# Kernel tuning notes

Hardware: AMD Instinct MI355X
Metric: run time of the kernel (lower is better)

## Reference

```python
import jax, jax.numpy as jnp
import numpy as np

B, P, N, C = 8, 4, 512, 768
H = 12
HD = C // H  # 64
SCALE = HD ** -0.5


def setup_inputs() -> dict:
    key = jax.random.key(0)
    k1, k2, k3 = jax.random.split(key, 3)
    x = jax.random.normal(k1, (B, P, N, C), dtype=jnp.float32)
    W_qkv = jax.random.normal(k2, (3 * C, C), dtype=jnp.float32) * (C ** -0.5)
    W_proj = jax.random.normal(k3, (C, C), dtype=jnp.float32) * (C ** -0.5)
    b_proj = jnp.zeros((C,), dtype=jnp.float32)
    return {"x": x, "W_qkv": W_qkv, "W_proj": W_proj, "b_proj": b_proj}


def reference(x, W_qkv, W_proj, b_proj):
    b, p, n, c = x.shape
    # qkv projection (no bias): (B,P,N,3C) -> (B,P,N,3,H,HD)
    qkv = jnp.einsum('bpnc,dc->bpnd', x, W_qkv).reshape(b, p, n, 3, H, HD)
    # -> (3, B, P, H, N, HD)
    qkv = jnp.transpose(qkv, (3, 0, 1, 4, 2, 5))
    q, k, v = qkv[0], qkv[1], qkv[2]
    # scaled dot-product attention per (batch, patch, head)
    attn = jnp.einsum('bphnd,bphmd->bphnm', q * SCALE, k)
    attn = jax.nn.softmax(attn, axis=-1)
    out = jnp.einsum('bphnm,bphmd->bphnd', attn, v)
    # merge heads: (B,P,N,H,HD) -> (B,P,N,C)
    out = jnp.transpose(out, (0, 1, 3, 2, 4)).reshape(b, p, n, c)
    return jnp.einsum('bpnc,dc->bpnd', out, W_proj) + b_proj
```

## Files before the change

kernel.cpp:

```cpp
#include <hip/hip_runtime.h>

typedef __bf16 bf16x8 __attribute__((ext_vector_type(8)));
typedef unsigned short u16x8 __attribute__((ext_vector_type(8)));
typedef float f32x4 __attribute__((ext_vector_type(4)));

#define GLOAD_LDS16(GP, LP)                                                        \
  __builtin_amdgcn_global_load_lds((const __attribute__((address_space(1))) void*)(GP), \
                                   (__attribute__((address_space(3))) void*)(LP), 16, 0, 0)

__device__ __forceinline__ unsigned short f2bf(float f) {
  unsigned int u = __builtin_bit_cast(unsigned int, f);
  u += 0x7FFFu + ((u >> 16) & 1u);
  return (unsigned short)(u >> 16);
}
__device__ __forceinline__ bf16x8 ldfrag(const unsigned short* p) {
  return __builtin_bit_cast(bf16x8, *(const u16x8*)p);
}
__device__ __forceinline__ f32x4 mfma16(bf16x8 a, bf16x8 b, f32x4 c) {
  return __builtin_amdgcn_mfma_f32_16x16x32_bf16(a, b, c, 0, 0, 0);
}

#define MTOK   16384
#define CDIM   768
#define C3     2304
#define C2     1536
#define NX     12582912
#define NQW    1769472
#define NPW    589824

#define XB_OFF    0ul
#define WQKV_OFF  25165824ul
#define WPROJ_OFF 28704768ul
#define QK_OFF    29884416ul
#define VT_OFF    80216064ul

__global__ __launch_bounds__(256) void convert_kernel(
    const float* __restrict__ x, const float* __restrict__ wqkv,
    const float* __restrict__ wproj, unsigned short* __restrict__ xb,
    unsigned short* __restrict__ wqkvb, unsigned short* __restrict__ wprojb) {
  const int NX4 = NX / 4, NQ4 = NQW / 4, NP4 = NPW / 4;
  const int total = NX4 + NQ4 + NP4;
  for (int i = blockIdx.x * 256 + threadIdx.x; i < total; i += gridDim.x * 256) {
    const float4* src; unsigned short* dst; float scale = 1.f; int j;
    if (i < NX4) { src = (const float4*)x; dst = xb; j = i; }
    else if (i < NX4 + NQ4) {
      j = i - NX4; src = (const float4*)wqkv; dst = wqkvb;
      int d = (j * 4) / CDIM; if (d < CDIM) scale = 0.125f;
    } else { j = i - NX4 - NQ4; src = (const float4*)wproj; dst = wprojb; }
    float4 v = src[j];
    unsigned int lo = f2bf(v.x * scale) | ((unsigned)f2bf(v.y * scale) << 16);
    unsigned int hi = f2bf(v.z * scale) | ((unsigned)f2bf(v.w * scale) << 16);
    uint2 pk; pk.x = lo; pk.y = hi;
    *(uint2*)(dst + (long)j * 4) = pk;
  }
}

template <int MODE>
__global__ __launch_bounds__(256) void gemm_bt(
    const unsigned short* __restrict__ A, const unsigned short* __restrict__ B,
    int K, int Nout,
    unsigned short* __restrict__ out_qk, unsigned short* __restrict__ out_vT,
    float* __restrict__ out_f32, const float* __restrict__ bias) {
  __shared__ unsigned short As[128 * 32];
  __shared__ unsigned short Bs[128 * 32];
  const int tid = threadIdx.x;
  const int wave = tid >> 6, lane = tid & 63;
  const int wy = wave >> 1, wx = wave & 1;
  const int l15 = lane & 15, quad = lane >> 4;
  const int bm = blockIdx.x, bn = blockIdx.y;

  f32x4 acc[4][4];
  for (int i = 0; i < 4; i++)
    for (int j = 0; j < 4; j++) acc[i][j] = f32x4{0.f, 0.f, 0.f, 0.f};

  const long Abase = (long)bm * 128 * K;
  const long Bbase = (long)bn * 128 * K;

  for (int kk = 0; kk < K; kk += 32) {
    for (int i = 0; i < 2; i++) {
      int c = wave * 128 + i * 64 + lane;
      int row = c >> 2, c16 = c & 3;
      GLOAD_LDS16(A + Abase + (long)row * K + kk + c16 * 8, As + c * 8);
      GLOAD_LDS16(B + Bbase + (long)row * K + kk + c16 * 8, Bs + c * 8);
    }
    __syncthreads();
    bf16x8 af[4], bfr[4];
    for (int mt = 0; mt < 4; mt++) af[mt]  = ldfrag(As + (wy * 64 + mt * 16 + l15) * 32 + quad * 8);
    for (int nt = 0; nt < 4; nt++) bfr[nt] = ldfrag(Bs + (wx * 64 + nt * 16 + l15) * 32 + quad * 8);
    for (int mt = 0; mt < 4; mt++)
      for (int nt = 0; nt < 4; nt++)
        acc[mt][nt] = mfma16(af[mt], bfr[nt], acc[mt][nt]);
    __syncthreads();
  }

  if (MODE == 0) {
    if (bn < 12) {
      for (int mt = 0; mt < 4; mt++) {
        int mg = bm * 128 + wy * 64 + mt * 16 + quad * 4;
        for (int nt = 0; nt < 4; nt++) {
          int d = bn * 128 + wx * 64 + nt * 16 + l15;
          for (int r = 0; r < 4; r++)
            out_qk[(long)(mg + r) * C2 + d] = f2bf(acc[mt][nt][r]);
        }
      }
    } else {
      for (int mt = 0; mt < 4; mt++) {
        int mg = bm * 128 + wy * 64 + mt * 16 + quad * 4;
        int bp = mg >> 9, n0 = mg & 511;
        for (int nt = 0; nt < 4; nt++) {
          int dp = bn * 128 - C2 + wx * 64 + nt * 16 + l15;
          int hh = dp >> 6, e = dp & 63;
          unsigned int lo = f2bf(acc[mt][nt][0]) | ((unsigned)f2bf(acc[mt][nt][1]) << 16);
          unsigned int hi = f2bf(acc[mt][nt][2]) | ((unsigned)f2bf(acc[mt][nt][3]) << 16);
          uint2 pk; pk.x = lo; pk.y = hi;
          *(uint2*)(out_vT + ((long)((bp * 12 + hh) * 64 + e) * 512 + n0)) = pk;
        }
      }
    }
  } else {
    for (int nt = 0; nt < 4; nt++) {
      int d = bn * 128 + wx * 64 + nt * 16 + l15;
      float bv = bias[d];
      for (int mt = 0; mt < 4; mt++) {
        int mg = bm * 128 + wy * 64 + mt * 16 + quad * 4;
        for (int r = 0; r < 4; r++)
          out_f32[(long)(mg + r) * Nout + d] = acc[mt][nt][r] + bv;
      }
    }
  }
}

__global__ __launch_bounds__(256) void attn_kernel(
    const unsigned short* __restrict__ qk, const unsigned short* __restrict__ vT,
    unsigned short* __restrict__ aout) {
  const int bph = blockIdx.x;
  const int qt  = blockIdx.y;
  const int bp = bph / 12, h = bph % 12;
  const int tid = threadIdx.x;
  const int wave = tid >> 6, lane = tid & 63;
  const int l15 = lane & 15, quad = lane >> 4;

  __shared__ unsigned short Qs[128 * 72];
  __shared__ unsigned short Ks[64 * 72];
  __shared__ unsigned short Vs[64 * 72];
  __shared__ unsigned short Ps[4 * 32 * 72];

  const unsigned short* Qg = qk + (long)(bp * 512 + qt * 128) * C2 + h * 64;
  const unsigned short* Kg = qk + (long)(bp * 512) * C2 + CDIM + h * 64;
  const unsigned short* Vg = vT + (long)(bp * 12 + h) * 64 * 512;

  for (int i = 0; i < 4; i++) {
    int c = tid + i * 256;
    int row = c >> 3, c8 = c & 7;
    *(uint4*)(Qs + row * 72 + c8 * 8) = *(const uint4*)(Qg + (long)row * C2 + c8 * 8);
  }

  f32x4 o[2][4];
  float mrow[2][4], lrow[2][4];
  for (int a = 0; a < 2; a++)
    for (int b = 0; b < 4; b++) o[a][b] = f32x4{0.f, 0.f, 0.f, 0.f};
  for (int a = 0; a < 2; a++)
    for (int r = 0; r < 4; r++) { mrow[a][r] = -1e30f; lrow[a][r] = 0.f; }

  for (int ch = 0; ch < 8; ch++) {
    if (ch) __syncthreads();
    for (int i = 0; i < 2; i++) {
      int c = tid + i * 256;
      int row = c >> 3, c8 = c & 7;
      *(uint4*)(Ks + row * 72 + c8 * 8) = *(const uint4*)(Kg + (long)(ch * 64 + row) * C2 + c8 * 8);
      *(uint4*)(Vs + row * 72 + c8 * 8) = *(const uint4*)(Vg + (long)row * 512 + ch * 64 + c8 * 8);
    }
    __syncthreads();

    f32x4 s[2][4];
    for (int a = 0; a < 2; a++)
      for (int b = 0; b < 4; b++) s[a][b] = f32x4{0.f, 0.f, 0.f, 0.f};
    for (int ks = 0; ks < 2; ks++) {
      bf16x8 a0 = ldfrag(Qs + (wave * 32 +      l15) * 72 + ks * 32 + quad * 8);
      bf16x8 a1 = ldfrag(Qs + (wave * 32 + 16 + l15) * 72 + ks * 32 + quad * 8);
      for (int nt = 0; nt < 4; nt++) {
        bf16x8 kb = ldfrag(Ks + (nt * 16 + l15) * 72 + ks * 32 + quad * 8);
        s[0][nt] = mfma16(a0, kb, s[0][nt]);
        s[1][nt] = mfma16(a1, kb, s[1][nt]);
      }
    }

    for (int mt2 = 0; mt2 < 2; mt2++) {
      for (int r = 0; r < 4; r++) {
        float mx = fmaxf(fmaxf(s[mt2][0][r], s[mt2][1][r]), fmaxf(s[mt2][2][r], s[mt2][3][r]));
        for (int off = 1; off < 16; off <<= 1) mx = fmaxf(mx, __shfl_xor(mx, off));
        float mnew = fmaxf(mrow[mt2][r], mx);
        float alpha = __expf(mrow[mt2][r] - mnew);
        mrow[mt2][r] = mnew;
        float rs = 0.f;
        for (int nt = 0; nt < 4; nt++) {
          float p = __expf(s[mt2][nt][r] - mnew);
          s[mt2][nt][r] = p;
          rs += p;
        }
        for (int off = 1; off < 16; off <<= 1) rs += __shfl_xor(rs, off);
        lrow[mt2][r] = lrow[mt2][r] * alpha + rs;
        for (int et = 0; et < 4; et++) o[mt2][et][r] *= alpha;
        for (int nt = 0; nt < 4; nt++)
          Ps[(wave * 32 + mt2 * 16 + quad * 4 + r) * 72 + nt * 16 + l15] = f2bf(s[mt2][nt][r]);
      }
    }

    for (int ks = 0; ks < 2; ks++) {
      bf16x8 p0 = ldfrag(Ps + (wave * 32 +      l15) * 72 + ks * 32 + quad * 8);
      bf16x8 p1 = ldfrag(Ps + (wave * 32 + 16 + l15) * 72 + ks * 32 + quad * 8);
      for (int et = 0; et < 4; et++) {
        bf16x8 vb = ldfrag(Vs + (et * 16 + l15) * 72 + ks * 32 + quad * 8);
        o[0][et] = mfma16(p0, vb, o[0][et]);
        o[1][et] = mfma16(p1, vb, o[1][et]);
      }
    }
  }

  for (int mt2 = 0; mt2 < 2; mt2++)
    for (int et = 0; et < 4; et++)
      for (int r = 0; r < 4; r++) {
        int nout = qt * 128 + wave * 32 + mt2 * 16 + quad * 4 + r;
        float v = o[mt2][et][r] / lrow[mt2][r];
        aout[(long)(bp * 512 + nout) * CDIM + h * 64 + et * 16 + l15] = f2bf(v);
      }
}

extern "C" void kernel_launch(void* const* d_in, const int* in_sizes, int n_in,
                              void* d_out, int out_size, void* d_ws, size_t ws_size,
                              hipStream_t stream) {
  (void)in_sizes; (void)n_in; (void)out_size; (void)ws_size;
  const float* x     = (const float*)d_in[0];
  const float* wqkv  = (const float*)d_in[1];
  const float* wproj = (const float*)d_in[2];
  const float* bproj = (const float*)d_in[3];
  float* out = (float*)d_out;
  char* ws = (char*)d_ws;

  unsigned short* xb     = (unsigned short*)(ws + XB_OFF);
  unsigned short* wqkvb  = (unsigned short*)(ws + WQKV_OFF);
  unsigned short* wprojb = (unsigned short*)(ws + WPROJ_OFF);
  unsigned short* qkbuf  = (unsigned short*)(ws + QK_OFF);
  unsigned short* vTbuf  = (unsigned short*)(ws + VT_OFF);
  unsigned short* attn_o = xb;

  convert_kernel<<<2048, 256, 0, stream>>>(x, wqkv, wproj, xb, wqkvb, wprojb);
  gemm_bt<0><<<dim3(128, 18), 256, 0, stream>>>(xb, wqkvb, CDIM, C3, qkbuf, vTbuf, nullptr, nullptr);
  attn_kernel<<<dim3(384, 4), 256, 0, stream>>>(qkbuf, vTbuf, attn_o);
  gemm_bt<1><<<dim3(128, 6), 256, 0, stream>>>(attn_o, wprojb, CDIM, CDIM, nullptr, nullptr, out, bproj);
}
```

Measured before the change: 309.1 us.

## Keep attention probabilities in registers via transposed S and 16x16x16 MFMA for PV

Computes S transposed (K as the A operand, Q as B) so each lane owns one query row. The P fragments can then feed the 16x16x16 bf16 MFMA for PV straight from registers, which removes the LDS round trip for P and the 16-lane shuffles in the row reductions. Softmax now uses exp2, with log2(e) folded into the Q weight scale, and the kernel adds a launch-bounds occupancy hint. The cost is running the PV product on the older, narrower MFMA instruction and higher register pressure.

```diff
diff --git a/kernel.cpp b/kernel.cpp
--- a/kernel.cpp
+++ b/kernel.cpp
@@ -2,6 +2,8 @@
 
 typedef __bf16 bf16x8 __attribute__((ext_vector_type(8)));
 typedef unsigned short u16x8 __attribute__((ext_vector_type(8)));
+typedef short s16x4 __attribute__((ext_vector_type(4)));
+typedef unsigned short u16x4 __attribute__((ext_vector_type(4)));
 typedef float f32x4 __attribute__((ext_vector_type(4)));
 
 #define GLOAD_LDS16(GP, LP)                                                        \
@@ -16,8 +18,14 @@
 __device__ __forceinline__ bf16x8 ldfrag(const unsigned short* p) {
   return __builtin_bit_cast(bf16x8, *(const u16x8*)p);
 }
+__device__ __forceinline__ s16x4 ldfrag4(const unsigned short* p) {
+  return __builtin_bit_cast(s16x4, *(const u16x4*)p);
+}
 __device__ __forceinline__ f32x4 mfma16(bf16x8 a, bf16x8 b, f32x4 c) {
   return __builtin_amdgcn_mfma_f32_16x16x32_bf16(a, b, c, 0, 0, 0);
+}
+__device__ __forceinline__ f32x4 mfma1k(s16x4 a, s16x4 b, f32x4 c) {
+  return __builtin_amdgcn_mfma_f32_16x16x16bf16_1k(a, b, c, 0, 0, 0);
 }
 
 #define MTOK   16384
@@ -27,6 +35,8 @@
 #define NX     12582912
 #define NQW    1769472
 #define NPW    589824
+
+#define QSCALE_LOG2E 0.1803368801111204f
 
 #define XB_OFF    0ul
 #define WQKV_OFF  25165824ul
@@ -45,7 +55,7 @@
     if (i < NX4) { src = (const float4*)x; dst = xb; j = i; }
     else if (i < NX4 + NQ4) {
       j = i - NX4; src = (const float4*)wqkv; dst = wqkvb;
-      int d = (j * 4) / CDIM; if (d < CDIM) scale = 0.125f;
+      int d = (j * 4) / CDIM; if (d < CDIM) scale = QSCALE_LOG2E;
     } else { j = i - NX4 - NQ4; src = (const float4*)wproj; dst = wprojb; }
     float4 v = src[j];
     unsigned int lo = f2bf(v.x * scale) | ((unsigned)f2bf(v.y * scale) << 16);
@@ -130,7 +140,7 @@
   }
 }
 
-__global__ __launch_bounds__(256) void attn_kernel(
+__global__ __launch_bounds__(256, 4) void attn_kernel(
     const unsigned short* __restrict__ qk, const unsigned short* __restrict__ vT,
     unsigned short* __restrict__ aout) {
   const int bph = blockIdx.x;
@@ -143,7 +153,6 @@
   __shared__ unsigned short Qs[128 * 72];
   __shared__ unsigned short Ks[64 * 72];
   __shared__ unsigned short Vs[64 * 72];
-  __shared__ unsigned short Ps[4 * 32 * 72];
 
   const unsigned short* Qg = qk + (long)(bp * 512 + qt * 128) * C2 + h * 64;
   const unsigned short* Kg = qk + (long)(bp * 512) * C2 + CDIM + h * 64;
@@ -156,11 +165,11 @@
   }
 
   f32x4 o[2][4];
-  float mrow[2][4], lrow[2][4];
-  for (int a = 0; a < 2; a++)
+  float mrow[2], lrow[2];
+  for (int a = 0; a < 2; a++) {
     for (int b = 0; b < 4; b++) o[a][b] = f32x4{0.f, 0.f, 0.f, 0.f};
-  for (int a = 0; a < 2; a++)
-    for (int r = 0; r < 4; r++) { mrow[a][r] = -1e30f; lrow[a][r] = 0.f; }
+    mrow[a] = -1e30f; lrow[a] = 0.f;
+  }
 
   for (int ch = 0; ch < 8; ch++) {
     if (ch) __syncthreads();
@@ -172,58 +181,65 @@
     }
     __syncthreads();
 
-    f32x4 s[2][4];
+    f32x4 st[2][4];
     for (int a = 0; a < 2; a++)
-      for (int b = 0; b < 4; b++) s[a][b] = f32x4{0.f, 0.f, 0.f, 0.f};
+      for (int b = 0; b < 4; b++) st[a][b] = f32x4{0.f, 0.f, 0.f, 0.f};
     for (int ks = 0; ks < 2; ks++) {
-      bf16x8 a0 = ldfrag(Qs + (wave * 32 +      l15) * 72 + ks * 32 + quad * 8);
-      bf16x8 a1 = ldfrag(Qs + (wave * 32 + 16 + l15) * 72 + ks * 32 + quad * 8);
+      bf16x8 qf[2];
+      qf[0] = ldfrag(Qs + (wave * 32 +      l15) * 72 + ks * 32 + quad * 8);
+      qf[1] = ldfrag(Qs + (wave * 32 + 16 + l15) * 72 + ks * 32 + quad * 8);
       for (int nt = 0; nt < 4; nt++) {
-        bf16x8 kb = ldfrag(Ks + (nt * 16 + l15) * 72 + ks * 32 + quad * 8);
-        s[0][nt] = mfma16(a0, kb, s[0][nt]);
-        s[1][nt] = mfma16(a1, kb, s[1][nt]);
-      }
-    }
-
+        bf16x8 kf = ldfrag(Ks + (nt * 16 + l15) * 72 + ks * 32 + quad * 8);
+        st[0][nt] = mfma16(kf, qf[0], st[0][nt]);
+        st[1][nt] = mfma16(kf, qf[1], st[1][nt]);
+      }
+    }
+
+    s16x4 pf[2][4];
     for (int mt2 = 0; mt2 < 2; mt2++) {
-      for (int r = 0; r < 4; r++) {
-        float mx = fmaxf(fmaxf(s[mt2][0][r], s[mt2][1][r]), fmaxf(s[mt2][2][r], s[mt2][3][r]));
-        for (int off = 1; off < 16; off <<= 1) mx = fmaxf(mx, __shfl_xor(mx, off));
-        float mnew = fmaxf(mrow[mt2][r], mx);
-        float alpha = __expf(mrow[mt2][r] - mnew);
-        mrow[mt2][r] = mnew;
-        float rs = 0.f;
-        for (int nt = 0; nt < 4; nt++) {
-          float p = __expf(s[mt2][nt][r] - mnew);
-          s[mt2][nt][r] = p;
-          rs += p;
+      float mx = -1e30f;
+      for (int nt = 0; nt < 4; nt++)
+        for (int r = 0; r < 4; r++) mx = fmaxf(mx, st[mt2][nt][r]);
+      mx = fmaxf(mx, __shfl_xor(mx, 16));
+      mx = fmaxf(mx, __shfl_xor(mx, 32));
+      float mnew = fmaxf(mrow[mt2], mx);
+      float alpha = __builtin_amdgcn_exp2f(mrow[mt2] - mnew);
+      mrow[mt2] = mnew;
+      float rs = 0.f;
+      for (int nt = 0; nt < 4; nt++) {
+        f32x4 p;
+        for (int r = 0; r < 4; r++) {
+          p[r] = __builtin_amdgcn_exp2f(st[mt2][nt][r] - mnew);
+          rs += p[r];
         }
-        for (int off = 1; off < 16; off <<= 1) rs += __shfl_xor(rs, off);
-        lrow[mt2][r] = lrow[mt2][r] * alpha + rs;
-        for (int et = 0; et < 4; et++) o[mt2][et][r] *= alpha;
-        for (int nt = 0; nt < 4; nt++)
-          Ps[(wave * 32 + mt2 * 16 + quad * 4 + r) * 72 + nt * 16 + l15] = f2bf(s[mt2][nt][r]);
-      }
-    }
-
-    for (int ks = 0; ks < 2; ks++) {
-      bf16x8 p0 = ldfrag(Ps + (wave * 32 +      l15) * 72 + ks * 32 + quad * 8);
-      bf16x8 p1 = ldfrag(Ps + (wave * 32 + 16 + l15) * 72 + ks * 32 + quad * 8);
+        s16x4 pk;
+        for (int r = 0; r < 4; r++) pk[r] = (short)f2bf(p[r]);
+        pf[mt2][nt] = pk;
+      }
+      rs += __shfl_xor(rs, 16);
+      rs += __shfl_xor(rs, 32);
+      lrow[mt2] = lrow[mt2] * alpha + rs;
+      for (int et = 0; et < 4; et++) o[mt2][et] *= alpha;
+    }
+
+    for (int nt = 0; nt < 4; nt++)
       for (int et = 0; et < 4; et++) {
-        bf16x8 vb = ldfrag(Vs + (et * 16 + l15) * 72 + ks * 32 + quad * 8);
-        o[0][et] = mfma16(p0, vb, o[0][et]);
-        o[1][et] = mfma16(p1, vb, o[1][et]);
-      }
-    }
-  }
-
-  for (int mt2 = 0; mt2 < 2; mt2++)
-    for (int et = 0; et < 4; et++)
-      for (int r = 0; r < 4; r++) {
-        int nout = qt * 128 + wave * 32 + mt2 * 16 + quad * 4 + r;
-        float v = o[mt2][et][r] / lrow[mt2][r];
-        aout[(long)(bp * 512 + nout) * CDIM + h * 64 + et * 16 + l15] = f2bf(v);
-      }
+        s16x4 vf = ldfrag4(Vs + (et * 16 + l15) * 72 + nt * 16 + quad * 4);
+        o[0][et] = mfma1k(vf, pf[0][nt], o[0][et]);
+        o[1][et] = mfma1k(vf, pf[1][nt], o[1][et]);
+      }
+  }
+
+  for (int mt2 = 0; mt2 < 2; mt2++) {
+    float inv = 1.f / lrow[mt2];
+    int q = qt * 128 + wave * 32 + mt2 * 16 + l15;
+    for (int et = 0; et < 4; et++) {
+      unsigned int lo = f2bf(o[mt2][et][0] * inv) | ((unsigned)f2bf(o[mt2][et][1] * inv) << 16);
+      unsigned int hi = f2bf(o[mt2][et][2] * inv) | ((unsigned)f2bf(o[mt2][et][3] * inv) << 16);
+      uint2 pk; pk.x = lo; pk.y = hi;
+      *(uint2*)(aout + (long)(bp * 512 + q) * CDIM + h * 64 + et * 16 + quad * 4) = pk;
+    }
+  }
 }
 
 extern "C" void kernel_launch(void* const* d_in, const int* in_sizes, int n_in,
```

After: 279.2 us. 1.11x faster.
